# Kernel optimization log

Measured on AMD Instinct MI355X. Metric: run time of the kernel, lower is better.

Reference implementation:

```python
import jax, jax.numpy as jnp
import numpy as np

D_MODEL = 512
N_HEADS = 8
HEAD_DIM = D_MODEL // N_HEADS
D_FF = 2048
EPS = 1e-5


def layer_norm(x, gamma, beta):
    mu = jnp.mean(x, axis=-1, keepdims=True)
    var = jnp.mean((x - mu) ** 2, axis=-1, keepdims=True)
    return (x - mu) * jax.lax.rsqrt(var + EPS) * gamma + beta


def setup_inputs() -> dict:
    key = jax.random.key(0)
    ks = jax.random.split(key, 17)
    B, S = 2, 2048
    s_in = 1.0 / np.sqrt(D_MODEL)
    s_ff = 1.0 / np.sqrt(D_FF)
    return {
        "x": jax.random.normal(ks[0], (B, S, D_MODEL), jnp.float32),
        "Wq": jax.random.normal(ks[1], (D_MODEL, D_MODEL), jnp.float32) * s_in,
        "bq": jnp.zeros((D_MODEL,), jnp.float32),
        "Wk": jax.random.normal(ks[2], (D_MODEL, D_MODEL), jnp.float32) * s_in,
        "bk": jnp.zeros((D_MODEL,), jnp.float32),
        "Wv": jax.random.normal(ks[3], (D_MODEL, D_MODEL), jnp.float32) * s_in,
        "bv": jnp.zeros((D_MODEL,), jnp.float32),
        "Wo": jax.random.normal(ks[4], (D_MODEL, D_MODEL), jnp.float32) * s_in,
        "bo": jnp.zeros((D_MODEL,), jnp.float32),
        "W1": jax.random.normal(ks[5], (D_MODEL, D_FF), jnp.float32) * s_in,
        "b1": jnp.zeros((D_FF,), jnp.float32),
        "W2": jax.random.normal(ks[6], (D_FF, D_MODEL), jnp.float32) * s_ff,
        "b2": jnp.zeros((D_MODEL,), jnp.float32),
        "g1": jnp.ones((D_MODEL,), jnp.float32),
        "be1": jnp.zeros((D_MODEL,), jnp.float32),
        "g2": jnp.ones((D_MODEL,), jnp.float32),
        "be2": jnp.zeros((D_MODEL,), jnp.float32),
    }


def reference(x, Wq, bq, Wk, bk, Wv, bv, Wo, bo, W1, b1, W2, b2, g1, be1, g2, be2):
    B, S, _ = x.shape
    # projections + split heads -> [B, H, S, Dh]
    def heads(t):
        return t.reshape(B, S, N_HEADS, HEAD_DIM).transpose(0, 2, 1, 3)
    q = heads(x @ Wq + bq)
    k = heads(x @ Wk + bk)
    v = heads(x @ Wv + bv)
    # explicit scaled dot-product attention (full [B,H,S,S] scores as in source)
    scores = jnp.einsum('bhqd,bhkd->bhqk', q, k) / np.sqrt(HEAD_DIM).astype(np.float32)
    attn = jax.nn.softmax(scores, axis=-1)
    ctx = jnp.einsum('bhqk,bhkd->bhqd', attn, v)
    ctx = ctx.transpose(0, 2, 1, 3).reshape(B, S, D_MODEL)
    attn_out = ctx @ Wo + bo
    # post-norm residual 1
    h = layer_norm(x + attn_out, g1, be1)
    # FFN
    ff = jax.nn.relu(h @ W1 + b1) @ W2 + b2
    # post-norm residual 2
    return layer_norm(h + ff, g2, be2)
```

## Files before the change

### kernel.cpp

```cpp
#include <hip/hip_runtime.h>
#include <cmath>

#define D_MODEL 512
#define N_HEADS 8
#define HEAD_DIM 64
#define D_FF 2048
#define SEQ 2048
#define BATCH 2
#define MROWS (BATCH * SEQ)

typedef __attribute__((ext_vector_type(8))) short short8;
typedef __attribute__((ext_vector_type(4))) float float4v;
typedef unsigned short ushort_t;

static __device__ __forceinline__ ushort_t f2bf(float f) {
    union { float f; unsigned u; } v; v.f = f;
    unsigned r = (v.u + 0x7FFFu + ((v.u >> 16) & 1u)) >> 16;
    return (ushort_t)r;
}
static __device__ __forceinline__ ushort_t f2bf_trunc(float f) {
    union { float f; unsigned u; } v; v.f = f;
    return (ushort_t)(v.u >> 16);
}

static __device__ __forceinline__ void gload16(const void* g, void* l) {
    __builtin_amdgcn_global_load_lds(
        (__attribute__((address_space(1))) void*)(unsigned long long)g,
        (__attribute__((address_space(3))) void*)(unsigned)(unsigned long long)l,
        16, 0, 0);
}

__global__ __launch_bounds__(256) void prep_k(
    const float* __restrict__ x,
    const float* __restrict__ Wq, const float* __restrict__ Wk,
    const float* __restrict__ Wv, const float* __restrict__ Wo,
    const float* __restrict__ W1, const float* __restrict__ W2,
    ushort_t* __restrict__ xb,
    ushort_t* __restrict__ WqkvT, ushort_t* __restrict__ WoT,
    ushort_t* __restrict__ W1T, ushort_t* __restrict__ W2T)
{
    int tile = blockIdx.x;
    if (tile >= 3072) {
        int i = (tile - 3072) * 256 + threadIdx.x;
        float4 f = ((const float4*)x)[i];
        ushort4 o;
        o.x = f2bf(f.x); o.y = f2bf(f.y); o.z = f2bf(f.z); o.w = f2bf(f.w);
        ((ushort4*)xb)[i] = o;
        return;
    }
    const float* src; ushort_t* dst; int Kd, Nd, tloc;
    if (tile < 1024) {
        int wsel = tile >> 8; tloc = tile & 255; Kd = 512; Nd = 512;
        if (wsel == 0)      { src = Wq; dst = WqkvT; }
        else if (wsel == 1) { src = Wk; dst = WqkvT + (size_t)512 * 512; }
        else if (wsel == 2) { src = Wv; dst = WqkvT + (size_t)1024 * 512; }
        else                { src = Wo; dst = WoT; }
    } else if (tile < 2048) { tloc = tile - 1024; Kd = 512;  Nd = 2048; src = W1; dst = W1T; }
    else                    { tloc = tile - 2048; Kd = 2048; Nd = 512;  src = W2; dst = W2T; }
    int tn = Nd >> 5;
    int k0 = (tloc / tn) << 5, n0 = (tloc % tn) << 5;
    __shared__ float tl[32][33];
    int c = threadIdx.x & 31, r = threadIdx.x >> 5;
    #pragma unroll
    for (int i = 0; i < 4; ++i)
        tl[r + i * 8][c] = src[(size_t)(k0 + r + i * 8) * Nd + n0 + c];
    __syncthreads();
    #pragma unroll
    for (int i = 0; i < 4; ++i)
        dst[(size_t)(n0 + r + i * 8) * Kd + k0 + c] = f2bf(tl[c][r + i * 8]);
}

template <int MODE>
__global__ __launch_bounds__(256) void gemm_std_k(
    const ushort_t* __restrict__ A, const ushort_t* __restrict__ BT,
    const float* __restrict__ bias, void* __restrict__ Cv,
    int N, int K, int Klen, size_t zstride)
{
    __shared__ ushort_t As[64 * 128];
    __shared__ ushort_t Bs[128 * 128];

    const int t = threadIdx.x;
    const int w = t >> 6, lane = t & 63, l16 = lane & 15, quad = lane >> 4;
    const int m0 = blockIdx.y * 64;
    const int n0 = blockIdx.x * 128;
    const int kbase = blockIdx.z * Klen;
    const int mbase = (w >> 1) * 32;
    const int nbase = (w & 1) * 64;
    const int lrow = lane >> 4;
    const int lchunk = lane & 15;

    float4v acc[2][4];
    #pragma unroll
    for (int mt = 0; mt < 2; ++mt)
        #pragma unroll
        for (int nt = 0; nt < 4; ++nt)
            acc[mt][nt] = (float4v){0.f, 0.f, 0.f, 0.f};

    for (int ks = kbase; ks < kbase + Klen; ks += 128) {
        __syncthreads();
        for (int c = w; c < 16; c += 4) {
            int rl = c * 4 + lrow;
            gload16(A + (size_t)(m0 + rl) * K + ks + ((lchunk ^ (rl & 7)) << 3),
                    &As[c * 512]);
        }
        for (int c = w; c < 32; c += 4) {
            int rl = c * 4 + lrow;
            gload16(BT + (size_t)(n0 + rl) * K + ks + ((lchunk ^ (rl & 7)) << 3),
                    &Bs[c * 512]);
        }
        __syncthreads();

        #pragma unroll
        for (int co = 0; co < 4; ++co) {
            const int poff = (((co * 4 + quad) ^ (l16 & 7)) << 3);
            short8 af[2], bf8[4];
            #pragma unroll
            for (int mt = 0; mt < 2; ++mt)
                af[mt] = *(const short8*)&As[(mbase + mt * 16 + l16) * 128 + poff];
            #pragma unroll
            for (int nt = 0; nt < 4; ++nt)
                bf8[nt] = *(const short8*)&Bs[(nbase + nt * 16 + l16) * 128 + poff];
            #pragma unroll
            for (int mt = 0; mt < 2; ++mt)
                #pragma unroll
                for (int nt = 0; nt < 4; ++nt)
                    acc[mt][nt] = __builtin_amdgcn_mfma_f32_16x16x32_bf16(
                        af[mt], bf8[nt], acc[mt][nt], 0, 0, 0);
        }
    }

    float* Cf = (float*)Cv + blockIdx.z * zstride;
    #pragma unroll
    for (int mt = 0; mt < 2; ++mt) {
        #pragma unroll
        for (int nt = 0; nt < 4; ++nt) {
            int gcol = n0 + nbase + nt * 16 + l16;
            float b = (MODE == 2) ? 0.f : bias[gcol];
            #pragma unroll
            for (int r = 0; r < 4; ++r) {
                int grow = m0 + mbase + mt * 16 + quad * 4 + r;
                float v = acc[mt][nt][r] + b;
                if (MODE == 1) v = fmaxf(v, 0.f);
                if (MODE == 1) ((ushort_t*)Cv)[(size_t)grow * N + gcol] = f2bf(v);
                else           Cf[(size_t)grow * N + gcol] = v;
            }
        }
    }
}

__global__ __launch_bounds__(256) void gemm_qkv_k(
    const ushort_t* __restrict__ A, const ushort_t* __restrict__ BT,
    const float* __restrict__ bq, const float* __restrict__ bk,
    const float* __restrict__ bv,
    ushort_t* __restrict__ Qb, ushort_t* __restrict__ Kb,
    ushort_t* __restrict__ VTb)
{
    __shared__ ushort_t As[64 * 128];
    __shared__ ushort_t Bs[128 * 128];

    const int t = threadIdx.x;
    const int w = t >> 6, lane = t & 63, l16 = lane & 15, quad = lane >> 4;
    const int m0 = blockIdx.y * 64;
    const int n0 = blockIdx.x * 128;
    const int mbase = (w >> 1) * 32;
    const int nbase = (w & 1) * 64;
    const int lrow = lane >> 4;
    const int lchunk = lane & 15;
    const int K = 512;

    float4v acc[2][4];
    #pragma unroll
    for (int mt = 0; mt < 2; ++mt)
        #pragma unroll
        for (int nt = 0; nt < 4; ++nt)
            acc[mt][nt] = (float4v){0.f, 0.f, 0.f, 0.f};

    for (int ks = 0; ks < 512; ks += 128) {
        __syncthreads();
        for (int c = w; c < 16; c += 4) {
            int rl = c * 4 + lrow;
            gload16(A + (size_t)(m0 + rl) * K + ks + ((lchunk ^ (rl & 7)) << 3),
                    &As[c * 512]);
        }
        for (int c = w; c < 32; c += 4) {
            int rl = c * 4 + lrow;
            gload16(BT + (size_t)(n0 + rl) * K + ks + ((lchunk ^ (rl & 7)) << 3),
                    &Bs[c * 512]);
        }
        __syncthreads();

        #pragma unroll
        for (int co = 0; co < 4; ++co) {
            const int poff = (((co * 4 + quad) ^ (l16 & 7)) << 3);
            short8 af[2], bf8[4];
            #pragma unroll
            for (int mt = 0; mt < 2; ++mt)
                af[mt] = *(const short8*)&As[(mbase + mt * 16 + l16) * 128 + poff];
            #pragma unroll
            for (int nt = 0; nt < 4; ++nt)
                bf8[nt] = *(const short8*)&Bs[(nbase + nt * 16 + l16) * 128 + poff];
            #pragma unroll
            for (int mt = 0; mt < 2; ++mt)
                #pragma unroll
                for (int nt = 0; nt < 4; ++nt)
                    acc[mt][nt] = __builtin_amdgcn_mfma_f32_16x16x32_bf16(
                        af[mt], bf8[nt], acc[mt][nt], 0, 0, 0);
        }
    }

    const int tsel = n0 >> 9;
    const float* bias = (tsel == 0) ? bq : (tsel == 1) ? bk : bv;
    const float scl = (tsel == 0) ? 0.18033688f : 1.0f;
    ushort_t* dst = (tsel == 0) ? Qb : Kb;

    #pragma unroll
    for (int mt = 0; mt < 2; ++mt) {
        #pragma unroll
        for (int nt = 0; nt < 4; ++nt) {
            int gcol = n0 + nbase + nt * 16 + l16;
            int lcol = gcol - (tsel << 9);
            int h = lcol >> 6, dh = lcol & 63;
            float b = bias[lcol];
            #pragma unroll
            for (int r = 0; r < 4; ++r) {
                int grow = m0 + mbase + mt * 16 + quad * 4 + r;
                int bb = grow >> 11, s = grow & 2047;
                float v = (acc[mt][nt][r] + b) * scl;
                if (tsel < 2)
                    dst[(((size_t)(bb * N_HEADS + h)) * SEQ + s) * HEAD_DIM + dh] = f2bf(v);
                else
                    VTb[(((size_t)(bb * N_HEADS + h)) * HEAD_DIM + dh) * SEQ + s] = f2bf(v);
            }
        }
    }
}

__global__ __launch_bounds__(256) void attn_mfma_k(
    const ushort_t* __restrict__ Qg, const ushort_t* __restrict__ Kg,
    const ushort_t* __restrict__ VTg,
    ushort_t* __restrict__ Ctx)
{
    __shared__ __align__(16) ushort_t Kbuf[4][64 * 64];
    __shared__ __align__(16) ushort_t Vbuf[4][64 * 64];
    __shared__ __align__(16) ushort_t Ps[4][16 * 64];

    const int bh = blockIdx.x;
    const int q0 = blockIdx.y * 64;
    const int t = threadIdx.x;
    const int w = t >> 6;
    const int lane = t & 63;
    const int l16 = lane & 15;
    const int quad = lane >> 4;
    const int qbase = q0 + w * 16;
    const float NM2 = -14.4269504f;

    const int r0 = t >> 3;
    const int r1 = r0 + 32;
    const int g0 = (t & 7) ^ (r0 & 7);
    const int g1 = (t & 7) ^ (r1 & 7);
    const size_t kgrow = (size_t)bh * SEQ;
    const size_t vgrow = (size_t)bh * HEAD_DIM;

#define ATTN_STAGE(b, kb)                                                       \
    {                                                                           \
        gload16(Kg + (kgrow + (kb) + r0) * HEAD_DIM + g0 * 8, &Kbuf[b][w * 512]);          \
        gload16(Kg + (kgrow + (kb) + r1) * HEAD_DIM + g1 * 8, &Kbuf[b][2048 + w * 512]);   \
        gload16(VTg + (vgrow + r0) * SEQ + (kb) + g0 * 8, &Vbuf[b][w * 512]);              \
        gload16(VTg + (vgrow + r1) * SEQ + (kb) + g1 * 8, &Vbuf[b][2048 + w * 512]);       \
    }

    short8 aq[2];
    {
        const ushort_t* qp = Qg + ((size_t)bh * SEQ + qbase + l16) * HEAD_DIM + quad * 8;
        aq[0] = *(const short8*)(qp);
        aq[1] = *(const short8*)(qp + 32);
    }

    const short8 ones8 = {(short)0x3F80, (short)0x3F80, (short)0x3F80, (short)0x3F80,
                          (short)0x3F80, (short)0x3F80, (short)0x3F80, (short)0x3F80};

    float4v o[4] = {};
    float4v ol = {};

    ATTN_STAGE(0, 0)
    ATTN_STAGE(1, 64)

    for (int i = 0; i < 32; ++i) {
        const int cur = i & 3;
        if (i < 30) {
            ATTN_STAGE((i + 2) & 3, (i + 2) * 64)
            asm volatile("s_waitcnt vmcnt(8)" ::: "memory");
        } else if (i == 30) {
            asm volatile("s_waitcnt vmcnt(4)" ::: "memory");
        } else {
            asm volatile("s_waitcnt vmcnt(0)" ::: "memory");
        }
        asm volatile("s_barrier" ::: "memory");

        const ushort_t* Kc = Kbuf[cur];
        const ushort_t* Vc = Vbuf[cur];

        float4v s[4];
        #pragma unroll
        for (int nt = 0; nt < 4; ++nt)
            s[nt] = (float4v){NM2, NM2, NM2, NM2};

        __builtin_amdgcn_s_setprio(1);
        #pragma unroll
        for (int c = 0; c < 2; ++c) {
            const int poff = (((c * 4 + quad) ^ (l16 & 7)) << 3);
            #pragma unroll
            for (int nt = 0; nt < 4; ++nt) {
                short8 bk8 = *(const short8*)&Kc[(nt * 16 + l16) * 64 + poff];
                s[nt] = __builtin_amdgcn_mfma_f32_16x16x32_bf16(aq[c], bk8, s[nt], 0, 0, 0);
            }
        }
        __builtin_amdgcn_s_setprio(0);

        #pragma unroll
        for (int nt = 0; nt < 4; ++nt)
            #pragma unroll
            for (int r = 0; r < 4; ++r)
                s[nt][r] = exp2f(s[nt][r]);

        #pragma unroll
        for (int nt = 0; nt < 4; ++nt)
            #pragma unroll
            for (int r = 0; r < 4; ++r) {
                int row = quad * 4 + r;
                int key = nt * 16 + l16;
                Ps[w][row * 64 + (((key >> 3) ^ (row & 7)) << 3) + (key & 7)] =
                    f2bf_trunc(s[nt][r]);
            }
        asm volatile("s_waitcnt lgkmcnt(0)" ::: "memory");

        __builtin_amdgcn_s_setprio(1);
        #pragma unroll
        for (int c = 0; c < 2; ++c) {
            short8 ap = *(const short8*)&Ps[w][l16 * 64 + ((((c << 2) + quad) ^ (l16 & 7)) << 3)];
            const int poff = (((c * 4 + quad) ^ (l16 & 7)) << 3);
            #pragma unroll
            for (int dt = 0; dt < 4; ++dt) {
                short8 bv8 = *(const short8*)&Vc[(dt * 16 + l16) * 64 + poff];
                o[dt] = __builtin_amdgcn_mfma_f32_16x16x32_bf16(ap, bv8, o[dt], 0, 0, 0);
            }
            ol = __builtin_amdgcn_mfma_f32_16x16x32_bf16(ap, ones8, ol, 0, 0, 0);
        }
        __builtin_amdgcn_s_setprio(0);
    }
#undef ATTN_STAGE

    const int bb = bh >> 3, hh = bh & 7;
    #pragma unroll
    for (int r = 0; r < 4; ++r) {
        int q = qbase + quad * 4 + r;
        float inv = 1.0f / ol[r];
        #pragma unroll
        for (int dt = 0; dt < 4; ++dt)
            Ctx[((size_t)(bb * SEQ + q)) * D_MODEL + hh * HEAD_DIM + dt * 16 + l16] =
                f2bf(o[dt][r] * inv);
    }
}

template <int WRITE_BF>
__global__ __launch_bounds__(256) void add_ln_k(
    const float* __restrict__ X, const float* __restrict__ P0,
    const float* __restrict__ P1, const float* __restrict__ bias,
    const float* __restrict__ gam, const float* __restrict__ bet,
    float* __restrict__ O, ushort_t* __restrict__ Ob)
{
    const int row = blockIdx.x;
    const int t = threadIdx.x;
    const size_t ro = (size_t)row * D_MODEL;

    float v0 = X[ro + t]       + P0[ro + t]       + P1[ro + t]       + bias[t];
    float v1 = X[ro + t + 256] + P0[ro + t + 256] + P1[ro + t + 256] + bias[t + 256];
    float s = v0 + v1;
    float ss = v0 * v0 + v1 * v1;
    #pragma unroll
    for (int off = 32; off > 0; off >>= 1) {
        s  += __shfl_down(s, off);
        ss += __shfl_down(ss, off);
    }
    __shared__ float sb[4], ssb[4];
    if ((t & 63) == 0) { sb[t >> 6] = s; ssb[t >> 6] = ss; }
    __syncthreads();
    float S  = sb[0] + sb[1] + sb[2] + sb[3];
    float SS = ssb[0] + ssb[1] + ssb[2] + ssb[3];
    float mu  = S * (1.0f / D_MODEL);
    float var = SS * (1.0f / D_MODEL) - mu * mu;
    float inv = rsqrtf(var + 1e-5f);
    float o0 = (v0 - mu) * inv * gam[t] + bet[t];
    float o1 = (v1 - mu) * inv * gam[t + 256] + bet[t + 256];
    O[ro + t]       = o0;
    O[ro + t + 256] = o1;
    if (WRITE_BF) {
        Ob[ro + t]       = f2bf(o0);
        Ob[ro + t + 256] = f2bf(o1);
    }
}

extern "C" void kernel_launch(void* const* d_in, const int* in_sizes, int n_in,
                              void* d_out, int out_size, void* d_ws, size_t ws_size,
                              hipStream_t stream)
{
    const float* x   = (const float*)d_in[0];
    const float* Wq  = (const float*)d_in[1];
    const float* bq  = (const float*)d_in[2];
    const float* Wk  = (const float*)d_in[3];
    const float* bk  = (const float*)d_in[4];
    const float* Wv  = (const float*)d_in[5];
    const float* bv  = (const float*)d_in[6];
    const float* Wo  = (const float*)d_in[7];
    const float* bo  = (const float*)d_in[8];
    const float* W1  = (const float*)d_in[9];
    const float* b1  = (const float*)d_in[10];
    const float* W2  = (const float*)d_in[11];
    const float* b2  = (const float*)d_in[12];
    const float* g1  = (const float*)d_in[13];
    const float* be1 = (const float*)d_in[14];
    const float* g2  = (const float*)d_in[15];
    const float* be2 = (const float*)d_in[16];
    float* out = (float*)d_out;
    float* ws  = (float*)d_ws;

    ushort_t* WoT   = (ushort_t*)(ws);
    ushort_t* W1T   = (ushort_t*)(ws + 131072);
    ushort_t* W2T   = (ushort_t*)(ws + 655360);
    ushort_t* WqkvT = (ushort_t*)(ws + 1179648);
    ushort_t* xb    = (ushort_t*)(ws + 1572864);
    ushort_t* Qb    = (ushort_t*)(ws + 2621440);
    ushort_t* Kb    = (ushort_t*)(ws + 3670016);
    ushort_t* VTb   = (ushort_t*)(ws + 4718592);
    ushort_t* Ctx   = (ushort_t*)(ws + 5767168);
    float*    Hh    = ws + 6881280;
    float*    P0    = ws + 8978432;
    float*    P1    = ws + 11075584;
    ushort_t* FF1   = (ushort_t*)(ws + 1572864);
    ushort_t* Hhb   = (ushort_t*)(ws + 5767168);

    prep_k<<<5120, 256, 0, stream>>>(x, Wq, Wk, Wv, Wo, W1, W2, xb, WqkvT, WoT, W1T, W2T);

    gemm_qkv_k<<<dim3(12, 64), 256, 0, stream>>>(xb, WqkvT, bq, bk, bv, Qb, Kb, VTb);

    attn_mfma_k<<<dim3(16, 32), 256, 0, stream>>>(Qb, Kb, VTb, Ctx);

    gemm_std_k<2><<<dim3(4, 64, 2), 256, 0, stream>>>(
        Ctx, WoT, nullptr, P0, 512, 512, 256, (size_t)MROWS * D_MODEL);

    add_ln_k<1><<<4096, 256, 0, stream>>>(x, P0, P1, bo, g1, be1, Hh, Hhb);

    gemm_std_k<1><<<dim3(16, 64), 256, 0, stream>>>(
        Hhb, W1T, b1, FF1, 2048, 512, 512, 0);

    gemm_std_k<2><<<dim3(4, 64, 2), 256, 0, stream>>>(
        FF1, W2T, nullptr, P0, 512, 2048, 1024, (size_t)MROWS * D_MODEL);

    add_ln_k<0><<<4096, 256, 0, stream>>>(Hh, P0, P1, b2, g2, be2, out, (ushort_t*)nullptr);
}
```

Measured before the change: 213.6 us.

## Fuse all stages into one cooperative persistent kernel with grid syncs

Replaces the eight separate kernel launches with a single cooperative kernel of 512 blocks. The kernel loops over the tiles of each stage (prep, QKV GEMM, attention, Wo GEMM, LN, FFN GEMMs, LN) and puts grid.sync between stages, with a union of shared-memory layouts. It keeps the original multi-launch path as a fallback if the cooperative launch fails. The aim is to remove per-launch overhead and inter-kernel gaps. In exchange, the grid is fixed at 512 blocks, which cuts parallelism for stages that had up to 5120 blocks. Occupancy is also tied to the largest shared-memory footprint, and grid syncs add cost.

Result: slower. 651.6 us (+205.0%).

```diff
diff --git a/kernel.cpp b/kernel.cpp
--- a/kernel.cpp
+++ b/kernel.cpp
@@ -1,5 +1,8 @@
 #include <hip/hip_runtime.h>
+#include <hip/hip_cooperative_groups.h>
 #include <cmath>
+
+namespace cg = cooperative_groups;
 
 #define D_MODEL 512
 #define N_HEADS 8
@@ -30,7 +33,19 @@
         16, 0, 0);
 }
 
-__global__ __launch_bounds__(256) void prep_k(
+struct SMemAttn { ushort_t K[4][4096]; ushort_t V[4][4096]; ushort_t P[4][1024]; };
+struct SMemGemm { ushort_t As[64 * 128]; ushort_t Bs[128 * 128]; };
+struct SMemPrep { float tl[32][33]; };
+struct SMemLn   { float sb[4]; float ssb[4]; };
+union SMem {
+    SMemAttn attn;
+    SMemGemm gemm;
+    SMemPrep prep;
+    SMemLn   ln;
+};
+
+static __device__ __forceinline__ void prep_tile(
+    SMem& sm, int tile, int t,
     const float* __restrict__ x,
     const float* __restrict__ Wq, const float* __restrict__ Wk,
     const float* __restrict__ Wv, const float* __restrict__ Wo,
@@ -39,9 +54,8 @@
     ushort_t* __restrict__ WqkvT, ushort_t* __restrict__ WoT,
     ushort_t* __restrict__ W1T, ushort_t* __restrict__ W2T)
 {
-    int tile = blockIdx.x;
     if (tile >= 3072) {
-        int i = (tile - 3072) * 256 + threadIdx.x;
+        int i = (tile - 3072) * 256 + t;
         float4 f = ((const float4*)x)[i];
         ushort4 o;
         o.x = f2bf(f.x); o.y = f2bf(f.y); o.z = f2bf(f.z); o.w = f2bf(f.w);
@@ -59,31 +73,26 @@
     else                    { tloc = tile - 2048; Kd = 2048; Nd = 512;  src = W2; dst = W2T; }
     int tn = Nd >> 5;
     int k0 = (tloc / tn) << 5, n0 = (tloc % tn) << 5;
-    __shared__ float tl[32][33];
-    int c = threadIdx.x & 31, r = threadIdx.x >> 5;
+    int c = t & 31, r = t >> 5;
     #pragma unroll
     for (int i = 0; i < 4; ++i)
-        tl[r + i * 8][c] = src[(size_t)(k0 + r + i * 8) * Nd + n0 + c];
+        sm.prep.tl[r + i * 8][c] = src[(size_t)(k0 + r + i * 8) * Nd + n0 + c];
     __syncthreads();
     #pragma unroll
     for (int i = 0; i < 4; ++i)
-        dst[(size_t)(n0 + r + i * 8) * Kd + k0 + c] = f2bf(tl[c][r + i * 8]);
+        dst[(size_t)(n0 + r + i * 8) * Kd + k0 + c] = f2bf(sm.prep.tl[c][r + i * 8]);
+    __syncthreads();
 }
 
 template <int MODE>
-__global__ __launch_bounds__(256) void gemm_std_k(
-    const ushort_t* __restrict__ A, const ushort_t* __restrict__ BT,
+static __device__ __forceinline__ void gemm_tile(
+    SMem& sm, int t, const ushort_t* __restrict__ A, const ushort_t* __restrict__ BT,
     const float* __restrict__ bias, void* __restrict__ Cv,
-    int N, int K, int Klen, size_t zstride)
-{
-    __shared__ ushort_t As[64 * 128];
-    __shared__ ushort_t Bs[128 * 128];
-
-    const int t = threadIdx.x;
+    int N, int K, int m0, int n0, int kbase, int Klen)
+{
+    ushort_t* As = sm.gemm.As;
+    ushort_t* Bs = sm.gemm.Bs;
     const int w = t >> 6, lane = t & 63, l16 = lane & 15, quad = lane >> 4;
-    const int m0 = blockIdx.y * 64;
-    const int n0 = blockIdx.x * 128;
-    const int kbase = blockIdx.z * Klen;
     const int mbase = (w >> 1) * 32;
     const int nbase = (w & 1) * 64;
     const int lrow = lane >> 4;
@@ -128,8 +137,9 @@
                         af[mt], bf8[nt], acc[mt][nt], 0, 0, 0);
         }
     }
-
-    float* Cf = (float*)Cv + blockIdx.z * zstride;
+    __syncthreads();
+
+    float* Cf = (float*)Cv;
     #pragma unroll
     for (int mt = 0; mt < 2; ++mt) {
         #pragma unroll
@@ -148,20 +158,17 @@
     }
 }
 
-__global__ __launch_bounds__(256) void gemm_qkv_k(
+static __device__ __forceinline__ void qkv_tile(
+    SMem& sm, int t, int m0, int n0,
     const ushort_t* __restrict__ A, const ushort_t* __restrict__ BT,
     const float* __restrict__ bq, const float* __restrict__ bk,
     const float* __restrict__ bv,
     ushort_t* __restrict__ Qb, ushort_t* __restrict__ Kb,
     ushort_t* __restrict__ VTb)
 {
-    __shared__ ushort_t As[64 * 128];
-    __shared__ ushort_t Bs[128 * 128];
-
-    const int t = threadIdx.x;
+    ushort_t* As = sm.gemm.As;
+    ushort_t* Bs = sm.gemm.Bs;
     const int w = t >> 6, lane = t & 63, l16 = lane & 15, quad = lane >> 4;
-    const int m0 = blockIdx.y * 64;
-    const int n0 = blockIdx.x * 128;
     const int mbase = (w >> 1) * 32;
     const int nbase = (w & 1) * 64;
     const int lrow = lane >> 4;
@@ -207,6 +214,7 @@
                         af[mt], bf8[nt], acc[mt][nt], 0, 0, 0);
         }
     }
+    __syncthreads();
 
     const int tsel = n0 >> 9;
     const float* bias = (tsel == 0) ? bq : (tsel == 1) ? bk : bv;
@@ -235,144 +243,15 @@
     }
 }
 
-__global__ __launch_bounds__(256) void attn_mfma_k(
-    const ushort_t* __restrict__ Qg, const ushort_t* __restrict__ Kg,
-    const ushort_t* __restrict__ VTg,
-    ushort_t* __restrict__ Ctx)
-{
-    __shared__ __align__(16) ushort_t Kbuf[4][64 * 64];
-    __shared__ __align__(16) ushort_t Vbuf[4][64 * 64];
-    __shared__ __align__(16) ushort_t Ps[4][16 * 64];
-
-    const int bh = blockIdx.x;
-    const int q0 = blockIdx.y * 64;
-    const int t = threadIdx.x;
-    const int w = t >> 6;
-    const int lane = t & 63;
-    const int l16 = lane & 15;
-    const int quad = lane >> 4;
-    const int qbase = q0 + w * 16;
-    const float NM2 = -14.4269504f;
-
-    const int r0 = t >> 3;
-    const int r1 = r0 + 32;
-    const int g0 = (t & 7) ^ (r0 & 7);
-    const int g1 = (t & 7) ^ (r1 & 7);
-    const size_t kgrow = (size_t)bh * SEQ;
-    const size_t vgrow = (size_t)bh * HEAD_DIM;
-
-#define ATTN_STAGE(b, kb)                                                       \
-    {                                                                           \
-        gload16(Kg + (kgrow + (kb) + r0) * HEAD_DIM + g0 * 8, &Kbuf[b][w * 512]);          \
-        gload16(Kg + (kgrow + (kb) + r1) * HEAD_DIM + g1 * 8, &Kbuf[b][2048 + w * 512]);   \
-        gload16(VTg + (vgrow + r0) * SEQ + (kb) + g0 * 8, &Vbuf[b][w * 512]);              \
-        gload16(VTg + (vgrow + r1) * SEQ + (kb) + g1 * 8, &Vbuf[b][2048 + w * 512]);       \
-    }
-
-    short8 aq[2];
-    {
-        const ushort_t* qp = Qg + ((size_t)bh * SEQ + qbase + l16) * HEAD_DIM + quad * 8;
-        aq[0] = *(const short8*)(qp);
-        aq[1] = *(const short8*)(qp + 32);
-    }
-
-    const short8 ones8 = {(short)0x3F80, (short)0x3F80, (short)0x3F80, (short)0x3F80,
-                          (short)0x3F80, (short)0x3F80, (short)0x3F80, (short)0x3F80};
-
-    float4v o[4] = {};
-    float4v ol = {};
-
-    ATTN_STAGE(0, 0)
-    ATTN_STAGE(1, 64)
-
-    for (int i = 0; i < 32; ++i) {
-        const int cur = i & 3;
-        if (i < 30) {
-            ATTN_STAGE((i + 2) & 3, (i + 2) * 64)
-            asm volatile("s_waitcnt vmcnt(8)" ::: "memory");
-        } else if (i == 30) {
-            asm volatile("s_waitcnt vmcnt(4)" ::: "memory");
-        } else {
-            asm volatile("s_waitcnt vmcnt(0)" ::: "memory");
-        }
-        asm volatile("s_barrier" ::: "memory");
-
-        const ushort_t* Kc = Kbuf[cur];
-        const ushort_t* Vc = Vbuf[cur];
-
-        float4v s[4];
-        #pragma unroll
-        for (int nt = 0; nt < 4; ++nt)
-            s[nt] = (float4v){NM2, NM2, NM2, NM2};
-
-        __builtin_amdgcn_s_setprio(1);
-        #pragma unroll
-        for (int c = 0; c < 2; ++c) {
-            const int poff = (((c * 4 + quad) ^ (l16 & 7)) << 3);
-            #pragma unroll
-            for (int nt = 0; nt < 4; ++nt) {
-                short8 bk8 = *(const short8*)&Kc[(nt * 16 + l16) * 64 + poff];
-                s[nt] = __builtin_amdgcn_mfma_f32_16x16x32_bf16(aq[c], bk8, s[nt], 0, 0, 0);
-            }
-        }
-        __builtin_amdgcn_s_setprio(0);
-
-        #pragma unroll
-        for (int nt = 0; nt < 4; ++nt)
-            #pragma unroll
-            for (int r = 0; r < 4; ++r)
-                s[nt][r] = exp2f(s[nt][r]);
-
-        #pragma unroll
-        for (int nt = 0; nt < 4; ++nt)
-            #pragma unroll
-            for (int r = 0; r < 4; ++r) {
-                int row = quad * 4 + r;
-                int key = nt * 16 + l16;
-                Ps[w][row * 64 + (((key >> 3) ^ (row & 7)) << 3) + (key & 7)] =
-                    f2bf_trunc(s[nt][r]);
-            }
-        asm volatile("s_waitcnt lgkmcnt(0)" ::: "memory");
-
-        __builtin_amdgcn_s_setprio(1);
-        #pragma unroll
-        for (int c = 0; c < 2; ++c) {
-            short8 ap = *(const short8*)&Ps[w][l16 * 64 + ((((c << 2) + quad) ^ (l16 & 7)) << 3)];
-            const int poff = (((c * 4 + quad) ^ (l16 & 7)) << 3);
-            #pragma unroll
-            for (int dt = 0; dt < 4; ++dt) {
-                short8 bv8 = *(const short8*)&Vc[(dt * 16 + l16) * 64 + poff];
-                o[dt] = __builtin_amdgcn_mfma_f32_16x16x32_bf16(ap, bv8, o[dt], 0, 0, 0);
-            }
-            ol = __builtin_amdgcn_mfma_f32_16x16x32_bf16(ap, ones8, ol, 0, 0, 0);
-        }
-        __builtin_amdgcn_s_setprio(0);
-    }
-#undef ATTN_STAGE
-
-    const int bb = bh >> 3, hh = bh & 7;
-    #pragma unroll
-    for (int r = 0; r < 4; ++r) {
-        int q = qbase + quad * 4 + r;
-        float inv = 1.0f / ol[r];
-        #pragma unroll
-        for (int dt = 0; dt < 4; ++dt)
-            Ctx[((size_t)(bb * SEQ + q)) * D_MODEL + hh * HEAD_DIM + dt * 16 + l16] =
-                f2bf(o[dt][r] * inv);
-    }
-}
-
 template <int WRITE_BF>
-__global__ __launch_bounds__(256) void add_ln_k(
+static __device__ __forceinline__ void ln_row(
+    SMem& sm, int row, int t,
     const float* __restrict__ X, const float* __restrict__ P0,
     const float* __restrict__ P1, const float* __restrict__ bias,
     const float* __restrict__ gam, const float* __restrict__ bet,
     float* __restrict__ O, ushort_t* __restrict__ Ob)
 {
-    const int row = blockIdx.x;
-    const int t = threadIdx.x;
     const size_t ro = (size_t)row * D_MODEL;
-
     float v0 = X[ro + t]       + P0[ro + t]       + P1[ro + t]       + bias[t];
     float v1 = X[ro + t + 256] + P0[ro + t + 256] + P1[ro + t + 256] + bias[t + 256];
     float s = v0 + v1;
@@ -382,11 +261,10 @@
         s  += __shfl_down(s, off);
         ss += __shfl_down(ss, off);
     }
-    __shared__ float sb[4], ssb[4];
-    if ((t & 63) == 0) { sb[t >> 6] = s; ssb[t >> 6] = ss; }
+    if ((t & 63) == 0) { sm.ln.sb[t >> 6] = s; sm.ln.ssb[t >> 6] = ss; }
     __syncthreads();
-    float S  = sb[0] + sb[1] + sb[2] + sb[3];
-    float SS = ssb[0] + ssb[1] + ssb[2] + ssb[3];
+    float S  = sm.ln.sb[0] + sm.ln.sb[1] + sm.ln.sb[2] + sm.ln.sb[3];
+    float SS = sm.ln.ssb[0] + sm.ln.ssb[1] + sm.ln.ssb[2] + sm.ln.ssb[3];
     float mu  = S * (1.0f / D_MODEL);
     float var = SS * (1.0f / D_MODEL) - mu * mu;
     float inv = rsqrtf(var + 1e-5f);
@@ -398,6 +276,368 @@
         Ob[ro + t]       = f2bf(o0);
         Ob[ro + t + 256] = f2bf(o1);
     }
+    __syncthreads();
+}
+
+__global__ __launch_bounds__(256) void mega_k(
+    const float* __restrict__ x,
+    const float* __restrict__ Wq, const float* __restrict__ bq,
+    const float* __restrict__ Wk, const float* __restrict__ bk,
+    const float* __restrict__ Wv, const float* __restrict__ bv,
+    const float* __restrict__ Wo, const float* __restrict__ bo,
+    const float* __restrict__ W1, const float* __restrict__ b1,
+    const float* __restrict__ W2, const float* __restrict__ b2,
+    const float* __restrict__ g1, const float* __restrict__ be1,
+    const float* __restrict__ g2, const float* __restrict__ be2,
+    float* __restrict__ out, float* __restrict__ ws)
+{
+    __shared__ SMem sm;
+    const int bid = blockIdx.x;
+    const int t = threadIdx.x;
+    cg::grid_group grid = cg::this_grid();
+
+    ushort_t* WoT   = (ushort_t*)(ws);
+    ushort_t* W1T   = (ushort_t*)(ws + 131072);
+    ushort_t* W2T   = (ushort_t*)(ws + 655360);
+    ushort_t* WqkvT = (ushort_t*)(ws + 1179648);
+    ushort_t* xb    = (ushort_t*)(ws + 1572864);
+    ushort_t* Qb    = (ushort_t*)(ws + 2621440);
+    ushort_t* Kb    = (ushort_t*)(ws + 3670016);
+    ushort_t* VTb   = (ushort_t*)(ws + 4718592);
+    ushort_t* Ctx   = (ushort_t*)(ws + 5767168);
+    float*    Hh    = ws + 6881280;
+    float*    P0    = ws + 8978432;
+    float*    P1    = ws + 11075584;
+    ushort_t* FF1   = (ushort_t*)(ws + 1572864);
+    ushort_t* Hhb   = (ushort_t*)(ws + 5767168);
+
+    for (int tile = bid; tile < 5120; tile += 512)
+        prep_tile(sm, tile, t, x, Wq, Wk, Wv, Wo, W1, W2, xb, WqkvT, WoT, W1T, W2T);
+    grid.sync();
+
+    for (int tile = bid; tile < 768; tile += 512)
+        qkv_tile(sm, t, (tile / 12) * 64, (tile % 12) * 128,
+                 xb, WqkvT, bq, bk, bv, Qb, Kb, VTb);
+    grid.sync();
+
+    {
+        const int bh = bid & 15;
+        const int q0 = (bid >> 4) * 64;
+        const int w = t >> 6;
+        const int lane = t & 63;
+        const int l16 = lane & 15;
+        const int quad = lane >> 4;
+        const int qbase = q0 + w * 16;
+        const float NM2 = -14.4269504f;
+
+        const int r0 = t >> 3;
+        const int r1 = r0 + 32;
+        const int g0 = (t & 7) ^ (r0 & 7);
+        const int g1 = (t & 7) ^ (r1 & 7);
+        const size_t kgrow = (size_t)bh * SEQ;
+        const size_t vgrow = (size_t)bh * HEAD_DIM;
+
+#define ATTN_STAGE(b, kb)                                                                     \
+    {                                                                                         \
+        gload16(Kb + (kgrow + (kb) + r0) * HEAD_DIM + g0 * 8, &sm.attn.K[b][w * 512]);        \
+        gload16(Kb + (kgrow + (kb) + r1) * HEAD_DIM + g1 * 8, &sm.attn.K[b][2048 + w * 512]); \
+        gload16(VTb + (vgrow + r0) * SEQ + (kb) + g0 * 8, &sm.attn.V[b][w * 512]);            \
+        gload16(VTb + (vgrow + r1) * SEQ + (kb) + g1 * 8, &sm.attn.V[b][2048 + w * 512]);     \
+    }
+
+        short8 aq[2];
+        {
+            const ushort_t* qp = Qb + ((size_t)bh * SEQ + qbase + l16) * HEAD_DIM + quad * 8;
+            aq[0] = *(const short8*)(qp);
+            aq[1] = *(const short8*)(qp + 32);
+        }
+
+        const short8 ones8 = {(short)0x3F80, (short)0x3F80, (short)0x3F80, (short)0x3F80,
+                              (short)0x3F80, (short)0x3F80, (short)0x3F80, (short)0x3F80};
+
+        float4v o[4] = {};
+        float4v ol = {};
+
+        ATTN_STAGE(0, 0)
+        ATTN_STAGE(1, 64)
+
+        for (int i = 0; i < 32; ++i) {
+            const int cur = i & 3;
+            if (i < 30) {
+                ATTN_STAGE((i + 2) & 3, (i + 2) * 64)
+                asm volatile("s_waitcnt vmcnt(8)" ::: "memory");
+            } else if (i == 30) {
+                asm volatile("s_waitcnt vmcnt(4)" ::: "memory");
+            } else {
+                asm volatile("s_waitcnt vmcnt(0)" ::: "memory");
+            }
+            asm volatile("s_barrier" ::: "memory");
+
+            const ushort_t* Kc = sm.attn.K[cur];
+            const ushort_t* Vc = sm.attn.V[cur];
+
+            float4v s[4];
+            #pragma unroll
+            for (int nt = 0; nt < 4; ++nt)
+                s[nt] = (float4v){NM2, NM2, NM2, NM2};
+
+            __builtin_amdgcn_s_setprio(1);
+            #pragma unroll
+            for (int c = 0; c < 2; ++c) {
+                const int poff = (((c * 4 + quad) ^ (l16 & 7)) << 3);
+                #pragma unroll
+                for (int nt = 0; nt < 4; ++nt) {
+                    short8 bk8 = *(const short8*)&Kc[(nt * 16 + l16) * 64 + poff];
+                    s[nt] = __builtin_amdgcn_mfma_f32_16x16x32_bf16(aq[c], bk8, s[nt], 0, 0, 0);
+                }
+            }
+            __builtin_amdgcn_s_setprio(0);
+
+            #pragma unroll
+            for (int nt = 0; nt < 4; ++nt)
+                #pragma unroll
+                for (int r = 0; r < 4; ++r)
+                    s[nt][r] = exp2f(s[nt][r]);
+
+            #pragma unroll
+            for (int nt = 0; nt < 4; ++nt)
+                #pragma unroll
+                for (int r = 0; r < 4; ++r) {
+                    int row = quad * 4 + r;
+                    int key = nt * 16 + l16;
+                    sm.attn.P[w][row * 64 + (((key >> 3) ^ (row & 7)) << 3) + (key & 7)] =
+                        f2bf_trunc(s[nt][r]);
+                }
+            asm volatile("s_waitcnt lgkmcnt(0)" ::: "memory");
+
+            __builtin_amdgcn_s_setprio(1);
+            #pragma unroll
+            for (int c = 0; c < 2; ++c) {
+                short8 ap = *(const short8*)
+                    &sm.attn.P[w][l16 * 64 + ((((c << 2) + quad) ^ (l16 & 7)) << 3)];
+                const int poff = (((c * 4 + quad) ^ (l16 & 7)) << 3);
+                #pragma unroll
+                for (int dt = 0; dt < 4; ++dt) {
+                    short8 bv8 = *(const short8*)&Vc[(dt * 16 + l16) * 64 + poff];
+                    o[dt] = __builtin_amdgcn_mfma_f32_16x16x32_bf16(ap, bv8, o[dt], 0, 0, 0);
+                }
+                ol = __builtin_amdgcn_mfma_f32_16x16x32_bf16(ap, ones8, ol, 0, 0, 0);
+            }
+            __builtin_amdgcn_s_setprio(0);
+        }
+#undef ATTN_STAGE
+
+        const int bb = bh >> 3, hh = bh & 7;
+        #pragma unroll
+        for (int r = 0; r < 4; ++r) {
+            int q = qbase + quad * 4 + r;
+            float inv = 1.0f / ol[r];
+            #pragma unroll
+            for (int dt = 0; dt < 4; ++dt)
+                Ctx[((size_t)(bb * SEQ + q)) * D_MODEL + hh * HEAD_DIM + dt * 16 + l16] =
+                    f2bf(o[dt][r] * inv);
+        }
+    }
+    grid.sync();
+
+    {
+        const int n0 = (bid & 3) * 128;
+        const int m0 = ((bid >> 2) & 63) * 64;
+        const int z  = bid >> 8;
+        gemm_tile<2>(sm, t, Ctx, WoT, nullptr, P0 + (size_t)z * 2097152,
+                     512, 512, m0, n0, z * 256, 256);
+    }
+    grid.sync();
+
+    for (int row = bid; row < 4096; row += 512)
+        ln_row<1>(sm, row, t, x, P0, P1, bo, g1, be1, Hh, Hhb);
+    grid.sync();
+
+    for (int tile = bid; tile < 1024; tile += 512)
+        gemm_tile<1>(sm, t, Hhb, W1T, b1, FF1,
+                     2048, 512, (tile >> 4) * 64, (tile & 15) * 128, 0, 512);
+    grid.sync();
+
+    {
+        const int n0 = (bid & 3) * 128;
+        const int m0 = ((bid >> 2) & 63) * 64;
+        const int z  = bid >> 8;
+        gemm_tile<2>(sm, t, FF1, W2T, nullptr, P0 + (size_t)z * 2097152,
+                     512, 2048, m0, n0, z * 1024, 1024);
+    }
+    grid.sync();
+
+    for (int row = bid; row < 4096; row += 512)
+        ln_row<0>(sm, row, t, Hh, P0, P1, b2, g2, be2, out, (ushort_t*)nullptr);
+}
+
+__global__ __launch_bounds__(256) void prep_k(
+    const float* __restrict__ x,
+    const float* __restrict__ Wq, const float* __restrict__ Wk,
+    const float* __restrict__ Wv, const float* __restrict__ Wo,
+    const float* __restrict__ W1, const float* __restrict__ W2,
+    ushort_t* __restrict__ xb,
+    ushort_t* __restrict__ WqkvT, ushort_t* __restrict__ WoT,
+    ushort_t* __restrict__ W1T, ushort_t* __restrict__ W2T)
+{
+    __shared__ SMem sm;
+    prep_tile(sm, blockIdx.x, threadIdx.x, x, Wq, Wk, Wv, Wo, W1, W2,
+              xb, WqkvT, WoT, W1T, W2T);
+}
+
+template <int MODE>
+__global__ __launch_bounds__(256) void gemm_std_k(
+    const ushort_t* __restrict__ A, const ushort_t* __restrict__ BT,
+    const float* __restrict__ bias, void* __restrict__ Cv,
+    int N, int K, int Klen, size_t zstride)
+{
+    __shared__ SMem sm;
+    void* Cvo = (MODE == 2) ? (void*)((float*)Cv + blockIdx.z * zstride) : Cv;
+    gemm_tile<MODE>(sm, threadIdx.x, A, BT, bias, Cvo, N, K,
+                    blockIdx.y * 64, blockIdx.x * 128, blockIdx.z * Klen, Klen);
+}
+
+__global__ __launch_bounds__(256) void gemm_qkv_k(
+    const ushort_t* __restrict__ A, const ushort_t* __restrict__ BT,
+    const float* __restrict__ bq, const float* __restrict__ bk,
+    const float* __restrict__ bv,
+    ushort_t* __restrict__ Qb, ushort_t* __restrict__ Kb,
+    ushort_t* __restrict__ VTb)
+{
+    __shared__ SMem sm;
+    qkv_tile(sm, threadIdx.x, blockIdx.y * 64, blockIdx.x * 128,
+             A, BT, bq, bk, bv, Qb, Kb, VTb);
+}
+
+__global__ __launch_bounds__(256) void attn_mfma_k(
+    const ushort_t* __restrict__ Qg, const ushort_t* __restrict__ Kg,
+    const ushort_t* __restrict__ VTg,
+    ushort_t* __restrict__ Ctx)
+{
+    __shared__ SMem sm;
+    const int bh = blockIdx.x;
+    const int q0 = blockIdx.y * 64;
+    const int t = threadIdx.x;
+    const int w = t >> 6;
+    const int lane = t & 63;
+    const int l16 = lane & 15;
+    const int quad = lane >> 4;
+    const int qbase = q0 + w * 16;
+    const float NM2 = -14.4269504f;
+
+    const int r0 = t >> 3;
+    const int r1 = r0 + 32;
+    const int g0 = (t & 7) ^ (r0 & 7);
+    const int g1 = (t & 7) ^ (r1 & 7);
+    const size_t kgrow = (size_t)bh * SEQ;
+    const size_t vgrow = (size_t)bh * HEAD_DIM;
+
+#define ATTN_STAGE(b, kb)                                                                     \
+    {                                                                                         \
+        gload16(Kg + (kgrow + (kb) + r0) * HEAD_DIM + g0 * 8, &sm.attn.K[b][w * 512]);        \
+        gload16(Kg + (kgrow + (kb) + r1) * HEAD_DIM + g1 * 8, &sm.attn.K[b][2048 + w * 512]); \
+        gload16(VTg + (vgrow + r0) * SEQ + (kb) + g0 * 8, &sm.attn.V[b][w * 512]);            \
+        gload16(VTg + (vgrow + r1) * SEQ + (kb) + g1 * 8, &sm.attn.V[b][2048 + w * 512]);     \
+    }
+
+    short8 aq[2];
+    {
+        const ushort_t* qp = Qg + ((size_t)bh * SEQ + qbase + l16) * HEAD_DIM + quad * 8;
+        aq[0] = *(const short8*)(qp);
+        aq[1] = *(const short8*)(qp + 32);
+    }
+    const short8 ones8 = {(short)0x3F80, (short)0x3F80, (short)0x3F80, (short)0x3F80,
+                          (short)0x3F80, (short)0x3F80, (short)0x3F80, (short)0x3F80};
+    float4v o[4] = {};
+    float4v ol = {};
+
+    ATTN_STAGE(0, 0)
+    ATTN_STAGE(1, 64)
+    for (int i = 0; i < 32; ++i) {
+        const int cur = i & 3;
+        if (i < 30) {
+            ATTN_STAGE((i + 2) & 3, (i + 2) * 64)
+            asm volatile("s_waitcnt vmcnt(8)" ::: "memory");
+        } else if (i == 30) {
+            asm volatile("s_waitcnt vmcnt(4)" ::: "memory");
+        } else {
+            asm volatile("s_waitcnt vmcnt(0)" ::: "memory");
+        }
+        asm volatile("s_barrier" ::: "memory");
+
+        const ushort_t* Kc = sm.attn.K[cur];
+        const ushort_t* Vc = sm.attn.V[cur];
+        float4v s[4];
+        #pragma unroll
+        for (int nt = 0; nt < 4; ++nt) s[nt] = (float4v){NM2, NM2, NM2, NM2};
+
+        __builtin_amdgcn_s_setprio(1);
+        #pragma unroll
+        for (int c = 0; c < 2; ++c) {
+            const int poff = (((c * 4 + quad) ^ (l16 & 7)) << 3);
+            #pragma unroll
+            for (int nt = 0; nt < 4; ++nt) {
+                short8 bk8 = *(const short8*)&Kc[(nt * 16 + l16) * 64 + poff];
+                s[nt] = __builtin_amdgcn_mfma_f32_16x16x32_bf16(aq[c], bk8, s[nt], 0, 0, 0);
+            }
+        }
+        __builtin_amdgcn_s_setprio(0);
+
+        #pragma unroll
+        for (int nt = 0; nt < 4; ++nt)
+            #pragma unroll
+            for (int r = 0; r < 4; ++r)
+                s[nt][r] = exp2f(s[nt][r]);
+
+        #pragma unroll
+        for (int nt = 0; nt < 4; ++nt)
+            #pragma unroll
+            for (int r = 0; r < 4; ++r) {
+                int row = quad * 4 + r;
+                int key = nt * 16 + l16;
+                sm.attn.P[w][row * 64 + (((key >> 3) ^ (row & 7)) << 3) + (key & 7)] =
+                    f2bf_trunc(s[nt][r]);
+            }
+        asm volatile("s_waitcnt lgkmcnt(0)" ::: "memory");
+
+        __builtin_amdgcn_s_setprio(1);
+        #pragma unroll
+        for (int c = 0; c < 2; ++c) {
+            short8 ap = *(const short8*)
+                &sm.attn.P[w][l16 * 64 + ((((c << 2) + quad) ^ (l16 & 7)) << 3)];
+            const int poff = (((c * 4 + quad) ^ (l16 & 7)) << 3);
+            #pragma unroll
+            for (int dt = 0; dt < 4; ++dt) {
+                short8 bv8 = *(const short8*)&Vc[(dt * 16 + l16) * 64 + poff];
+                o[dt] = __builtin_amdgcn_mfma_f32_16x16x32_bf16(ap, bv8, o[dt], 0, 0, 0);
+            }
+            ol = __builtin_amdgcn_mfma_f32_16x16x32_bf16(ap, ones8, ol, 0, 0, 0);
+        }
+        __builtin_amdgcn_s_setprio(0);
+    }
+#undef ATTN_STAGE
+
+    const int bb = bh >> 3, hh = bh & 7;
+    #pragma unroll
+    for (int r = 0; r < 4; ++r) {
+        int q = qbase + quad * 4 + r;
+        float inv = 1.0f / ol[r];
+        #pragma unroll
+        for (int dt = 0; dt < 4; ++dt)
+            Ctx[((size_t)(bb * SEQ + q)) * D_MODEL + hh * HEAD_DIM + dt * 16 + l16] =
+                f2bf(o[dt][r] * inv);
+    }
+}
+
+template <int WRITE_BF>
+__global__ __launch_bounds__(256) void add_ln_k(
+    const float* __restrict__ X, const float* __restrict__ P0,
+    const float* __restrict__ P1, const float* __restrict__ bias,
+    const float* __restrict__ gam, const float* __restrict__ bet,
+    float* __restrict__ O, ushort_t* __restrict__ Ob)
+{
+    __shared__ SMem sm;
+    ln_row<WRITE_BF>(sm, blockIdx.x, threadIdx.x, X, P0, P1, bias, gam, bet, O, Ob);
 }
 
 extern "C" void kernel_launch(void* const* d_in, const int* in_sizes, int n_in,
@@ -424,37 +664,44 @@
     float* out = (float*)d_out;
     float* ws  = (float*)d_ws;
 
-    ushort_t* WoT   = (ushort_t*)(ws);
-    ushort_t* W1T   = (ushort_t*)(ws + 131072);
-    ushort_t* W2T   = (ushort_t*)(ws + 655360);
-    ushort_t* WqkvT = (ushort_t*)(ws + 1179648);
-    ushort_t* xb    = (ushort_t*)(ws + 1572864);
-    ushort_t* Qb    = (ushort_t*)(ws + 2621440);
-    ushort_t* Kb    = (ushort_t*)(ws + 3670016);
-    ushort_t* VTb   = (ushort_t*)(ws + 4718592);
-    ushort_t* Ctx   = (ushort_t*)(ws + 5767168);
-    float*    Hh    = ws + 6881280;
-    float*    P0    = ws + 8978432;
-    float*    P1    = ws + 11075584;
-    ushort_t* FF1   = (ushort_t*)(ws + 1572864);
-    ushort_t* Hhb   = (ushort_t*)(ws + 5767168);
-
-    prep_k<<<5120, 256, 0, stream>>>(x, Wq, Wk, Wv, Wo, W1, W2, xb, WqkvT, WoT, W1T, W2T);
-
-    gemm_qkv_k<<<dim3(12, 64), 256, 0, stream>>>(xb, WqkvT, bq, bk, bv, Qb, Kb, VTb);
-
-    attn_mfma_k<<<dim3(16, 32), 256, 0, stream>>>(Qb, Kb, VTb, Ctx);
-
-    gemm_std_k<2><<<dim3(4, 64, 2), 256, 0, stream>>>(
-        Ctx, WoT, nullptr, P0, 512, 512, 256, (size_t)MROWS * D_MODEL);
-
-    add_ln_k<1><<<4096, 256, 0, stream>>>(x, P0, P1, bo, g1, be1, Hh, Hhb);
-
-    gemm_std_k<1><<<dim3(16, 64), 256, 0, stream>>>(
-        Hhb, W1T, b1, FF1, 2048, 512, 512, 0);
-
-    gemm_std_k<2><<<dim3(4, 64, 2), 256, 0, stream>>>(
-        FF1, W2T, nullptr, P0, 512, 2048, 1024, (size_t)MROWS * D_MODEL);
-
-    add_ln_k<0><<<4096, 256, 0, stream>>>(Hh, P0, P1, b2, g2, be2, out, (ushort_t*)nullptr);
-}
+    void* args[] = {
+        (void*)&x,  (void*)&Wq, (void*)&bq, (void*)&Wk, (void*)&bk,
+        (void*)&Wv, (void*)&bv, (void*)&Wo, (void*)&bo,
+        (void*)&W1, (void*)&b1, (void*)&W2, (void*)&b2,
+        (void*)&g1, (void*)&be1, (void*)&g2, (void*)&be2,
+        (void*)&out, (void*)&ws };
+
+    hipError_t err = hipLaunchCooperativeKernel(
+        (void*)mega_k, dim3(512), dim3(256), args, 0, stream);
+
+    if (err != hipSuccess) {
+        ushort_t* WoT   = (ushort_t*)(ws);
+        ushort_t* W1T   = (ushort_t*)(ws + 131072);
+        ushort_t* W2T   = (ushort_t*)(ws + 655360);
+        ushort_t* WqkvT = (ushort_t*)(ws + 1179648);
+        ushort_t* xb    = (ushort_t*)(ws + 1572864);
+        ushort_t* Qb    = (ushort_t*)(ws + 2621440);
+        ushort_t* Kb    = (ushort_t*)(ws + 3670016);
+        ushort_t* VTb   = (ushort_t*)(ws + 4718592);
+        ushort_t* Ctx   = (ushort_t*)(ws + 5767168);
+        float*    Hh    = ws + 6881280;
+        float*    P0    = ws + 8978432;
+        float*    P1    = ws + 11075584;
+        ushort_t* FF1   = (ushort_t*)(ws + 1572864);
+        ushort_t* Hhb   = (ushort_t*)(ws + 5767168);
+
+        prep_k<<<5120, 256, 0, stream>>>(x, Wq, Wk, Wv, Wo, W1, W2,
+                                         xb, WqkvT, WoT, W1T, W2T);
+        gemm_qkv_k<<<dim3(12, 64), 256, 0, stream>>>(xb, WqkvT, bq, bk, bv, Qb, Kb, VTb);
+        attn_mfma_k<<<dim3(16, 32), 256, 0, stream>>>(Qb, Kb, VTb, Ctx);
+        gemm_std_k<2><<<dim3(4, 64, 2), 256, 0, stream>>>(
+            Ctx, WoT, nullptr, P0, 512, 512, 256, (size_t)MROWS * D_MODEL);
+        add_ln_k<1><<<4096, 256, 0, stream>>>(x, P0, P1, bo, g1, be1, Hh, Hhb);
+        gemm_std_k<1><<<dim3(16, 64), 256, 0, stream>>>(
+            Hhb, W1T, b1, FF1, 2048, 512, 512, 0);
+        gemm_std_k<2><<<dim3(4, 64, 2), 256, 0, stream>>>(
+            FF1, W2T, nullptr, P0, 512, 2048, 1024, (size_t)MROWS * D_MODEL);
+        add_ln_k<0><<<4096, 256, 0, stream>>>(Hh, P0, P1, b2, g2, be2, out,
+                                              (ushort_t*)nullptr);
+    }
+}
```

## Fuse Wo projection GEMM with residual add and LayerNorm

Applied to the files above, without the earlier changes.

Replaces the split-K Wo GEMM plus the separate add+LayerNorm kernel with one kernel. Each block computes a full 16-row by 512-column output tile, so it can apply the bias, the residual and the LayerNorm in registers using shuffle and shared-memory reductions. This removes the fp32 partial-sum round trip through global memory and one launch. In exchange the grid shrinks to 256 blocks that each hold a lot of shared memory (about 144KB), which lowers occupancy. Each block also re-streams the whole Wo weight matrix, and variance is now computed as E[x^2]-mu^2.

Measured after the change: 209.5 us. Within noise of the previous version (-1.9%).

```diff
diff --git a/kernel.cpp b/kernel.cpp
--- a/kernel.cpp
+++ b/kernel.cpp
@@ -359,6 +359,121 @@
         for (int dt = 0; dt < 4; ++dt)
             Ctx[((size_t)(bb * SEQ + q)) * D_MODEL + hh * HEAD_DIM + dt * 16 + l16] =
                 f2bf(o[dt][r] * inv);
+    }
+}
+
+__global__ __launch_bounds__(256) void wo_ln_k(
+    const ushort_t* __restrict__ Ctx,
+    const ushort_t* __restrict__ WoT,
+    const float* __restrict__ x,
+    const float* __restrict__ bo,
+    const float* __restrict__ gam, const float* __restrict__ bet,
+    float* __restrict__ Hh, ushort_t* __restrict__ Hhb)
+{
+    __shared__ __align__(16) ushort_t As[16 * 512];
+    __shared__ __align__(16) ushort_t Bs[2][512 * 64];
+    __shared__ float red[2][4][16];
+
+    const int t = threadIdx.x;
+    const int w = t >> 6, lane = t & 63, l16 = lane & 15, quad = lane >> 4;
+    const int m0 = blockIdx.x * 16;
+    const int K = 512;
+
+    #pragma unroll
+    for (int p = 0; p < 4; ++p) {
+        int row = p * 4 + w;
+        int g = (lane & 56) | ((lane & 7) ^ (row & 7));
+        gload16(Ctx + (size_t)(m0 + row) * K + g * 8, &As[row * 512]);
+    }
+
+#define WOLN_STAGE_B(b, ks)                                                     \
+    {                                                                           \
+        _Pragma("unroll")                                                       \
+        for (int c = 0; c < 16; ++c) {                                          \
+            int row = c * 32 + (t >> 3);                                        \
+            int g = (t & 7) ^ (row & 7);                                        \
+            gload16(WoT + (size_t)row * K + (ks) * 64 + g * 8,                  \
+                    &Bs[b][c * 2048 + w * 512]);                                \
+        }                                                                       \
+    }
+
+    float4v acc[8];
+    #pragma unroll
+    for (int nt = 0; nt < 8; ++nt) acc[nt] = (float4v){0.f, 0.f, 0.f, 0.f};
+
+    WOLN_STAGE_B(0, 0)
+
+    for (int ks = 0; ks < 8; ++ks) {
+        const int cur = ks & 1;
+        if (ks < 7) {
+            WOLN_STAGE_B(cur ^ 1, ks + 1)
+            asm volatile("s_waitcnt vmcnt(16)" ::: "memory");
+        } else {
+            asm volatile("s_waitcnt vmcnt(0)" ::: "memory");
+        }
+        asm volatile("s_barrier" ::: "memory");
+
+        #pragma unroll
+        for (int c = 0; c < 2; ++c) {
+            const int poff = (((c * 4 + quad) ^ (l16 & 7)) << 3);
+            short8 af = *(const short8*)&As[l16 * 512 + ks * 64 + poff];
+            #pragma unroll
+            for (int nt = 0; nt < 8; ++nt) {
+                short8 bv = *(const short8*)&Bs[cur][(w * 128 + nt * 16 + l16) * 64 + poff];
+                acc[nt] = __builtin_amdgcn_mfma_f32_16x16x32_bf16(af, bv, acc[nt], 0, 0, 0);
+            }
+        }
+        asm volatile("s_barrier" ::: "memory");
+    }
+#undef WOLN_STAGE_B
+
+    float v[8][4];
+    float s[4] = {0.f, 0.f, 0.f, 0.f}, ss[4] = {0.f, 0.f, 0.f, 0.f};
+    #pragma unroll
+    for (int nt = 0; nt < 8; ++nt) {
+        int col = w * 128 + nt * 16 + l16;
+        float b = bo[col];
+        #pragma unroll
+        for (int r = 0; r < 4; ++r) {
+            int grow = m0 + quad * 4 + r;
+            float val = acc[nt][r] + b + x[(size_t)grow * D_MODEL + col];
+            v[nt][r] = val;
+            s[r] += val;
+            ss[r] += val * val;
+        }
+    }
+    #pragma unroll
+    for (int r = 0; r < 4; ++r) {
+        #pragma unroll
+        for (int m = 1; m < 16; m <<= 1) {
+            s[r]  += __shfl_xor(s[r], m);
+            ss[r] += __shfl_xor(ss[r], m);
+        }
+    }
+    if (l16 == 0) {
+        #pragma unroll
+        for (int r = 0; r < 4; ++r) {
+            red[0][w][quad * 4 + r] = s[r];
+            red[1][w][quad * 4 + r] = ss[r];
+        }
+    }
+    __syncthreads();
+    #pragma unroll
+    for (int r = 0; r < 4; ++r) {
+        int lrow = quad * 4 + r;
+        float S  = red[0][0][lrow] + red[0][1][lrow] + red[0][2][lrow] + red[0][3][lrow];
+        float SS = red[1][0][lrow] + red[1][1][lrow] + red[1][2][lrow] + red[1][3][lrow];
+        float mu  = S * (1.0f / D_MODEL);
+        float var = SS * (1.0f / D_MODEL) - mu * mu;
+        float inv = rsqrtf(var + 1e-5f);
+        int grow = m0 + lrow;
+        #pragma unroll
+        for (int nt = 0; nt < 8; ++nt) {
+            int col = w * 128 + nt * 16 + l16;
+            float o = (v[nt][r] - mu) * inv * gam[col] + bet[col];
+            Hh[(size_t)grow * D_MODEL + col] = o;
+            Hhb[(size_t)grow * D_MODEL + col] = f2bf(o);
+        }
     }
 }
 
@@ -445,10 +560,7 @@
 
     attn_mfma_k<<<dim3(16, 32), 256, 0, stream>>>(Qb, Kb, VTb, Ctx);
 
-    gemm_std_k<2><<<dim3(4, 64, 2), 256, 0, stream>>>(
-        Ctx, WoT, nullptr, P0, 512, 512, 256, (size_t)MROWS * D_MODEL);
-
-    add_ln_k<1><<<4096, 256, 0, stream>>>(x, P0, P1, bo, g1, be1, Hh, Hhb);
+    wo_ln_k<<<256, 256, 0, stream>>>(Ctx, WoT, x, bo, g1, be1, Hh, Hhb);
 
     gemm_std_k<1><<<dim3(16, 64), 256, 0, stream>>>(
         Hhb, W1T, b1, FF1, 2048, 512, 512, 0);
```
